# Performance work log

Hardware: AMD Instinct MI355X
Metric: run time of the kernel (lower is better)

The kernel has to match this reference:

```python
import jax, jax.numpy as jnp
import numpy as np

N_NODES = 50000
N_EDGES = 800000
N_RELS = 200
D = 128


def setup_inputs() -> dict:
    key = jax.random.key(0)
    ks = jax.random.split(key, 9)
    h = jax.random.normal(ks[0], (N_NODES, D), dtype=jnp.float32)
    r = jax.random.normal(ks[1], (N_RELS, D), dtype=jnp.float32)
    norm = jax.random.uniform(ks[2], (N_NODES, 1), dtype=jnp.float32)
    src = jax.random.randint(ks[3], (N_EDGES,), 0, N_NODES, dtype=jnp.int32)
    dst = jax.random.randint(ks[4], (N_EDGES,), 0, N_NODES, dtype=jnp.int32)
    rel = jax.random.randint(ks[5], (N_EDGES,), 0, N_RELS, dtype=jnp.int32)
    stdv = 1.0 / np.sqrt(D)
    W_msg = jax.random.uniform(ks[6], (D, D), minval=-stdv, maxval=stdv, dtype=jnp.float32)
    W = jax.random.uniform(ks[7], (D, D), minval=-stdv, maxval=stdv, dtype=jnp.float32)
    b = jax.random.uniform(ks[8], (D,), minval=-stdv, maxval=stdv, dtype=jnp.float32)
    return {"h": h, "r": r, "norm": norm, "src": src, "dst": dst, "rel": rel,
            "W_msg": W_msg, "W": W, "b": b}


def reference(h, r, norm, src, dst, rel, W_msg, W, b):
    # dropout=0.0 (eval); h = h * norm (symmetric-norm pre-scale)
    hn = h * norm                                    # [N, D]
    # per-edge message: (h_src - r_rel) @ W_msg
    msg = (hn[src] - r[rel]) @ W_msg                 # [E, D]
    # scatter-sum to destination nodes, then post-scale by norm
    agg = jax.ops.segment_sum(msg, dst, num_segments=hn.shape[0]) * norm  # [N, D]
    out = hn @ W + agg + b
    return jax.nn.relu(out)
```

## Files before the change

### kernel.cpp

```cpp
#include <hip/hip_runtime.h>

#define N_NODES 50000
#define N_EDGES 800000
#define DIM 128
#define K2 256
#define GN 64
#define NBUCK 196
#define EPB 4096
#define BCAP 16384

typedef unsigned short u16;
typedef __attribute__((ext_vector_type(8))) short short8;
typedef __attribute__((ext_vector_type(4))) float f32x4;

__device__ __forceinline__ float bf2f(u16 v) {
    union { unsigned int u; float f; } x;
    x.u = ((unsigned int)v) << 16;
    return x.f;
}

__device__ __forceinline__ u16 f2bf(float f) {
    union { unsigned int u; float f; } x;
    x.f = f;
    return (u16)((x.u + 0x7FFFu + ((x.u >> 16) & 1u)) >> 16);
}

__global__ void detect_kernel(const void* hraw, int* flag) {
    __shared__ int cnt;
    if (threadIdx.x == 0) cnt = 0;
    __syncthreads();
    const u16* p = (const u16*)hraw;
    u16 v = p[2 * threadIdx.x];
    float a = fabsf(bf2f(v));
    int insane = ((v & 0x7F80) == 0x7F80) || (a != 0.0f && (a > 1e6f || a < 1e-20f));
    if (insane) atomicAdd(&cnt, 1);
    __syncthreads();
    if (threadIdx.x == 0) flag[0] = (cnt > 64) ? 1 : 0;
}

#define PREP_H (N_NODES * 32)
#define PREP_R (200 * 32)
#define PREP_W 8192
__global__ __launch_bounds__(256) void prep_kernel(
    const void* __restrict__ h, const void* __restrict__ r, const void* __restrict__ norm,
    const void* __restrict__ W, const void* __restrict__ Wmsg,
    u16* __restrict__ hx, u16* __restrict__ r_bf, u16* __restrict__ wt,
    const int* __restrict__ flag)
{
    int t = blockIdx.x * 256 + threadIdx.x;
    int isf = flag[0];
    if (t < PREP_H) {
        int n = t >> 5, c = t & 31;
        float4 v; float nv;
        if (isf) {
            nv = ((const float*)norm)[n];
            v = *(const float4*)((const float*)h + (size_t)n * DIM + c * 4);
        } else {
            nv = bf2f(((const u16*)norm)[n]);
            ushort4 u = *(const ushort4*)((const u16*)h + (size_t)n * DIM + c * 4);
            v = make_float4(bf2f(u.x), bf2f(u.y), bf2f(u.z), bf2f(u.w));
        }
        ushort4 o;
        o.x = f2bf(v.x * nv); o.y = f2bf(v.y * nv); o.z = f2bf(v.z * nv); o.w = f2bf(v.w * nv);
        *(ushort4*)(hx + (size_t)n * K2 + c * 4) = o;
    } else if (t < PREP_H + PREP_R) {
        int t2 = t - PREP_H;
        int rho = t2 >> 5, c = t2 & 31;
        float4 v;
        if (isf) v = *(const float4*)((const float*)r + (size_t)rho * DIM + c * 4);
        else {
            ushort4 u = *(const ushort4*)((const u16*)r + (size_t)rho * DIM + c * 4);
            v = make_float4(bf2f(u.x), bf2f(u.y), bf2f(u.z), bf2f(u.w));
        }
        ushort4 o;
        o.x = f2bf(v.x); o.y = f2bf(v.y); o.z = f2bf(v.z); o.w = f2bf(v.w);
        *(ushort4*)(r_bf + (size_t)rho * DIM + c * 4) = o;
    } else if (t < PREP_H + PREP_R + PREP_W) {
        int t3 = t - PREP_H - PREP_R;
        int j = t3 >> 6;
        int k0 = (t3 & 63) * 4;
        ushort4 o;
        u16* op = (u16*)&o;
        for (int kk = 0; kk < 4; ++kk) {
            int k = k0 + kk;
            float wv;
            if (isf) wv = (k < 128) ? ((const float*)W)[(size_t)k * DIM + j]
                                    : ((const float*)Wmsg)[(size_t)(k - 128) * DIM + j];
            else     wv = (k < 128) ? bf2f(((const u16*)W)[(size_t)k * DIM + j])
                                    : bf2f(((const u16*)Wmsg)[(size_t)(k - 128) * DIM + j]);
            op[kk] = f2bf(wv);
        }
        *(ushort4*)(wt + (size_t)j * K2 + k0) = o;
    }
}

__global__ __launch_bounds__(256) void coarse_hist(const int* __restrict__ dst, int* __restrict__ bucketCount) {
    __shared__ int hh[NBUCK];
    for (int i = threadIdx.x; i < NBUCK; i += 256) hh[i] = 0;
    __syncthreads();
    int stride = gridDim.x * 256;
    for (int e = blockIdx.x * 256 + threadIdx.x; e < N_EDGES; e += stride)
        atomicAdd(&hh[dst[e] >> 8], 1);
    __syncthreads();
    for (int i = threadIdx.x; i < NBUCK; i += 256)
        if (hh[i]) atomicAdd(&bucketCount[i], hh[i]);
}

__global__ void bucket_scan(const int* __restrict__ bucketCount,
                            int* __restrict__ bucketBase, int* __restrict__ bucketCursor) {
    __shared__ int sd[256];
    int t = threadIdx.x;
    int c = (t < NBUCK) ? bucketCount[t] : 0;
    sd[t] = c;
    __syncthreads();
    for (int off = 1; off < 256; off <<= 1) {
        int v = (t >= off) ? sd[t - off] : 0;
        __syncthreads();
        sd[t] += v;
        __syncthreads();
    }
    if (t < NBUCK) { int ex = sd[t] - c; bucketBase[t] = ex; bucketCursor[t] = ex; }
    if (t == 0) bucketBase[NBUCK] = N_EDGES;
}

__global__ __launch_bounds__(512) void fill_lds(
    const int* __restrict__ dst, const int* __restrict__ src, const int* __restrict__ rel,
    int* __restrict__ bucketCursor, int* __restrict__ spk)
{
    __shared__ int hist[NBUCK];
    __shared__ int lbase[NBUCK];
    __shared__ int gbase[NBUCK];
    __shared__ int sd[256];
    __shared__ int pay[EPB];
    __shared__ unsigned char bkt[EPB];
    int tid = threadIdx.x;
    for (int i = tid; i < NBUCK; i += 512) hist[i] = 0;
    __syncthreads();
    int e0 = blockIdx.x * EPB;
    int myb[8], myr[8], myp[8];
#pragma unroll
    for (int i = 0; i < 8; ++i) {
        int e = e0 + i * 512 + tid;
        myb[i] = -1;
        if (e < N_EDGES) {
            int d = dst[e];
            int b = d >> 8;
            myb[i] = b;
            myr[i] = atomicAdd(&hist[b], 1);
            myp[i] = src[e] | (rel[e] << 16) | ((d & 255) << 24);
        }
    }
    __syncthreads();
    if (tid < 256) sd[tid] = (tid < NBUCK) ? hist[tid] : 0;
    __syncthreads();
    for (int off = 1; off < 256; off <<= 1) {
        int v = 0;
        if (tid < 256 && tid >= off) v = sd[tid - off];
        __syncthreads();
        if (tid < 256) sd[tid] += v;
        __syncthreads();
    }
    if (tid < NBUCK) {
        lbase[tid] = sd[tid] - hist[tid];
        gbase[tid] = hist[tid] ? atomicAdd(&bucketCursor[tid], hist[tid]) : 0;
    }
    __syncthreads();
#pragma unroll
    for (int i = 0; i < 8; ++i) {
        if (myb[i] >= 0) {
            int lp = lbase[myb[i]] + myr[i];
            pay[lp] = myp[i];
            bkt[lp] = (unsigned char)myb[i];
        }
    }
    __syncthreads();
    int total = N_EDGES - e0; if (total > EPB) total = EPB;
#pragma unroll
    for (int i = 0; i < 8; ++i) {
        int lp = i * 512 + tid;
        if (lp < total) {
            int b = bkt[lp];
            spk[gbase[b] + (lp - lbase[b])] = pay[lp];
        }
    }
}

__global__ __launch_bounds__(256) void node_sort(
    const int* __restrict__ bucketBase, int* __restrict__ spk, int* __restrict__ cursor)
{
    __shared__ int stage[BCAP];
    __shared__ int hist[256];
    __shared__ int nbase[256];
    __shared__ int sd[256];
    int b = blockIdx.x;
    int base = bucketBase[b], end = bucketBase[b + 1];
    int size = end - base; if (size > BCAP) size = BCAP;
    int t = threadIdx.x;
    hist[t] = 0;
    __syncthreads();
    for (int i = t; i < size; i += 256) {
        int pk = spk[base + i];
        stage[i] = pk;
        atomicAdd(&hist[(pk >> 24) & 255], 1);
    }
    __syncthreads();
    int c = hist[t];
    sd[t] = c;
    __syncthreads();
    for (int off = 1; off < 256; off <<= 1) {
        int v = (t >= off) ? sd[t - off] : 0;
        __syncthreads();
        sd[t] += v;
        __syncthreads();
    }
    nbase[t] = sd[t] - c;
    int node = b * 256 + t;
    if (node < N_NODES) cursor[node] = base + sd[t];
    hist[t] = 0;
    __syncthreads();
    for (int i = t; i < size; i += 256) {
        int pk = stage[i];
        int nd = (pk >> 24) & 255;
        int rk = atomicAdd(&hist[nd], 1);
        spk[base + nbase[nd] + rk] = pk;
    }
}

__global__ __launch_bounds__(256) void gather_kernel(
    u16* hx, const u16* __restrict__ r_bf, const void* __restrict__ norm,
    const int* __restrict__ cursor, const int* __restrict__ spk, const int* __restrict__ flag)
{
    int gid = blockIdx.x * 256 + threadIdx.x;
    int n = gid >> 4;
    int g = gid & 15;
    if (n >= N_NODES) return;
    int base = (n == 0) ? 0 : cursor[n - 1];
    int end = cursor[n];
    float acc[8] = {};
    for (int i0 = base; i0 < end; i0 += 16) {
        int my = i0 + g;
        int pk = (my < end) ? spk[my] : 0;
        int m = end - i0; if (m > 16) m = 16;
        int j = 0;
        for (; j + 1 < m; j += 2) {
            int pj0 = __shfl(pk, j, 16);
            int pj1 = __shfl(pk, j + 1, 16);
            int s0 = pj0 & 0xFFFF, r0 = (pj0 >> 16) & 0xFF;
            int s1 = pj1 & 0xFFFF, r1 = (pj1 >> 16) & 0xFF;
            short8 h0 = *(const short8*)(hx + (size_t)s0 * K2 + g * 8);
            short8 v0 = *(const short8*)(r_bf + (size_t)r0 * DIM + g * 8);
            short8 h1 = *(const short8*)(hx + (size_t)s1 * K2 + g * 8);
            short8 v1 = *(const short8*)(r_bf + (size_t)r1 * DIM + g * 8);
#pragma unroll
            for (int d = 0; d < 8; ++d)
                acc[d] += bf2f((u16)h0[d]) - bf2f((u16)v0[d]);
#pragma unroll
            for (int d = 0; d < 8; ++d)
                acc[d] += bf2f((u16)h1[d]) - bf2f((u16)v1[d]);
        }
        if (j < m) {
            int pj = __shfl(pk, j, 16);
            int s = pj & 0xFFFF, rl = (pj >> 16) & 0xFF;
            short8 hv = *(const short8*)(hx + (size_t)s * K2 + g * 8);
            short8 rv = *(const short8*)(r_bf + (size_t)rl * DIM + g * 8);
#pragma unroll
            for (int d = 0; d < 8; ++d)
                acc[d] += bf2f((u16)hv[d]) - bf2f((u16)rv[d]);
        }
    }
    float nv = flag[0] ? ((const float*)norm)[n] : bf2f(((const u16*)norm)[n]);
    short8 o;
#pragma unroll
    for (int d = 0; d < 8; ++d) o[d] = (short)f2bf(acc[d] * nv);
    *(short8*)(hx + (size_t)n * K2 + 128 + g * 8) = o;
}

__global__ __launch_bounds__(256) void mfma_gemm(
    const u16* __restrict__ hx, const u16* __restrict__ wt,
    const void* __restrict__ bias, void* __restrict__ out, const int* __restrict__ flag)
{
    __shared__ u16 X[GN][264];
    int tid = threadIdx.x;
    int nblk = blockIdx.x * GN;

    for (int i = tid; i < GN * 32; i += 256) {
        int nl = i >> 5, c = i & 31;
        int n = nblk + nl;
        short8 v = {0, 0, 0, 0, 0, 0, 0, 0};
        if (n < N_NODES) v = *(const short8*)(hx + (size_t)n * K2 + c * 8);
        *(short8*)&X[nl][c * 8] = v;
    }
    __syncthreads();

    int w = tid >> 6, lane = tid & 63;
    int m = lane & 15, quad = lane >> 4;
    int row0 = w * 16;
    int isf = flag[0];

    short8 a[8];
#pragma unroll
    for (int kb = 0; kb < 8; ++kb)
        a[kb] = *(const short8*)&X[row0 + m][kb * 32 + quad * 8];

#pragma unroll
    for (int ct = 0; ct < 8; ++ct) {
        int n0 = ct * 16;
        f32x4 acc = {0.f, 0.f, 0.f, 0.f};
#pragma unroll
        for (int kb = 0; kb < 8; ++kb) {
            short8 bv = *(const short8*)(wt + (size_t)(n0 + m) * K2 + kb * 32 + quad * 8);
            acc = __builtin_amdgcn_mfma_f32_16x16x32_bf16(a[kb], bv, acc, 0, 0, 0);
        }
        int col = n0 + m;
        float bb = isf ? ((const float*)bias)[col] : bf2f(((const u16*)bias)[col]);
#pragma unroll
        for (int rg = 0; rg < 4; ++rg) {
            int n = nblk + row0 + quad * 4 + rg;
            if (n < N_NODES) {
                float v = acc[rg] + bb;
                v = v > 0.f ? v : 0.f;
                if (isf) ((float*)out)[(size_t)n * DIM + col] = v;
                else     ((u16*)out)[(size_t)n * DIM + col] = f2bf(v);
            }
        }
    }
}

static inline size_t alup(size_t x) { return (x + 255) & ~(size_t)255; }

extern "C" void kernel_launch(void* const* d_in, const int* in_sizes, int n_in,
                              void* d_out, int out_size, void* d_ws, size_t ws_size,
                              hipStream_t stream) {
    const void* h    = d_in[0];
    const void* r    = d_in[1];
    const void* norm = d_in[2];
    const int* src   = (const int*)d_in[3];
    const int* dst   = (const int*)d_in[4];
    const int* rel   = (const int*)d_in[5];
    const void* Wmsg = d_in[6];
    const void* W    = d_in[7];
    const void* b    = d_in[8];

    char* p = (char*)d_ws;
    int* flag     = (int*)p;                 p += 256;
    u16* hx       = (u16*)p;                 p += alup((size_t)N_NODES * K2 * 2);
    u16* r_bf     = (u16*)p;                 p += alup((size_t)200 * DIM * 2);
    u16* wt       = (u16*)p;                 p += alup((size_t)DIM * K2 * 2);
    int* cursor   = (int*)p;                 p += alup((size_t)N_NODES * 4);
    int* bucketCount  = (int*)p;             p += alup((size_t)NBUCK * 4);
    int* bucketBase   = (int*)p;             p += alup((size_t)(NBUCK + 1) * 4);
    int* bucketCursor = (int*)p;             p += alup((size_t)NBUCK * 4);
    int* spk      = (int*)p;                 p += alup((size_t)N_EDGES * 4);

    detect_kernel<<<1, 256, 0, stream>>>(h, flag);
    prep_kernel<<<(PREP_H + PREP_R + PREP_W + 255) / 256, 256, 0, stream>>>(
        h, r, norm, W, Wmsg, hx, r_bf, wt, flag);

    hipMemsetAsync(bucketCount, 0, (size_t)NBUCK * 4, stream);
    coarse_hist<<<128, 256, 0, stream>>>(dst, bucketCount);
    bucket_scan<<<1, 256, 0, stream>>>(bucketCount, bucketBase, bucketCursor);
    fill_lds<<<(N_EDGES + EPB - 1) / EPB, 512, 0, stream>>>(dst, src, rel, bucketCursor, spk);
    node_sort<<<NBUCK, 256, 0, stream>>>(bucketBase, spk, cursor);

    gather_kernel<<<(N_NODES * 16 + 255) / 256, 256, 0, stream>>>(hx, r_bf, norm, cursor, spk, flag);
    mfma_gemm<<<(N_NODES + GN - 1) / GN, 256, 0, stream>>>(hx, wt, b, d_out, flag);
}
```

Before: 198.4 us.

## Fuse detect/prep/hist kernels, inline dtype sniff, stage relation table in LDS

Removes the separate detect kernel by having each block sniff the input dtype with a wavefront ballot. The prep and coarse histogram kernels merge into one launch, and norm and bias are pre-converted to fixed formats. The gather kernel now uses 1024-thread blocks and copies the 200x128 bf16 relation table into LDS, replacing global loads of r with LDS reads. The aim is fewer launches and less global traffic, at the cost of a 51KB LDS load per block, which can lower occupancy.

```diff
diff --git a/kernel.cpp b/kernel.cpp
--- a/kernel.cpp
+++ b/kernel.cpp
@@ -5,6 +5,7 @@
 #define DIM 128
 #define K2 256
 #define GN 64
+#define NREL 200
 #define NBUCK 196
 #define EPB 4096
 #define BCAP 16384
@@ -25,30 +26,44 @@
     return (u16)((x.u + 0x7FFFu + ((x.u >> 16) & 1u)) >> 16);
 }
 
-__global__ void detect_kernel(const void* hraw, int* flag) {
-    __shared__ int cnt;
-    if (threadIdx.x == 0) cnt = 0;
-    __syncthreads();
-    const u16* p = (const u16*)hraw;
-    u16 v = p[2 * threadIdx.x];
+__device__ __forceinline__ int sniff_fp32(const void* h, int tid) {
+    const u16* hp = (const u16*)h;
+    u16 v = hp[2 * (tid & 63)];
     float a = fabsf(bf2f(v));
     int insane = ((v & 0x7F80) == 0x7F80) || (a != 0.0f && (a > 1e6f || a < 1e-20f));
-    if (insane) atomicAdd(&cnt, 1);
-    __syncthreads();
-    if (threadIdx.x == 0) flag[0] = (cnt > 64) ? 1 : 0;
+    return __popcll(__ballot(insane)) > 16;
 }
 
 #define PREP_H (N_NODES * 32)
-#define PREP_R (200 * 32)
+#define PREP_R (NREL * 32)
 #define PREP_W 8192
-__global__ __launch_bounds__(256) void prep_kernel(
+#define PREP_N (N_NODES / 4)
+#define PREP_B 32
+#define PREP_TOT (PREP_H + PREP_R + PREP_W + PREP_N + PREP_B)
+#define PREP_BLOCKS ((PREP_TOT + 255) / 256)
+#define HIST_BLOCKS 128
+__global__ __launch_bounds__(256) void prep_hist(
     const void* __restrict__ h, const void* __restrict__ r, const void* __restrict__ norm,
-    const void* __restrict__ W, const void* __restrict__ Wmsg,
+    const void* __restrict__ W, const void* __restrict__ Wmsg, const void* __restrict__ bias,
+    const int* __restrict__ dst,
     u16* __restrict__ hx, u16* __restrict__ r_bf, u16* __restrict__ wt,
-    const int* __restrict__ flag)
-{
-    int t = blockIdx.x * 256 + threadIdx.x;
-    int isf = flag[0];
+    u16* __restrict__ norm_bf, float* __restrict__ b_f, int* __restrict__ bucketCount)
+{
+    __shared__ int hh[NBUCK];
+    int tid = threadIdx.x;
+    if (blockIdx.x >= PREP_BLOCKS) {
+        for (int i = tid; i < NBUCK; i += 256) hh[i] = 0;
+        __syncthreads();
+        int stride = HIST_BLOCKS * 256;
+        for (int e = (blockIdx.x - PREP_BLOCKS) * 256 + tid; e < N_EDGES; e += stride)
+            atomicAdd(&hh[dst[e] >> 8], 1);
+        __syncthreads();
+        for (int i = tid; i < NBUCK; i += 256)
+            if (hh[i]) atomicAdd(&bucketCount[i], hh[i]);
+        return;
+    }
+    int isf = sniff_fp32(h, tid);
+    int t = blockIdx.x * 256 + tid;
     if (t < PREP_H) {
         int n = t >> 5, c = t & 31;
         float4 v; float nv;
@@ -91,19 +106,26 @@
             op[kk] = f2bf(wv);
         }
         *(ushort4*)(wt + (size_t)j * K2 + k0) = o;
-    }
-}
-
-__global__ __launch_bounds__(256) void coarse_hist(const int* __restrict__ dst, int* __restrict__ bucketCount) {
-    __shared__ int hh[NBUCK];
-    for (int i = threadIdx.x; i < NBUCK; i += 256) hh[i] = 0;
-    __syncthreads();
-    int stride = gridDim.x * 256;
-    for (int e = blockIdx.x * 256 + threadIdx.x; e < N_EDGES; e += stride)
-        atomicAdd(&hh[dst[e] >> 8], 1);
-    __syncthreads();
-    for (int i = threadIdx.x; i < NBUCK; i += 256)
-        if (hh[i]) atomicAdd(&bucketCount[i], hh[i]);
+    } else if (t < PREP_H + PREP_R + PREP_W + PREP_N) {
+        int n0 = (t - PREP_H - PREP_R - PREP_W) * 4;
+        ushort4 o;
+        if (isf) {
+            float4 v = *(const float4*)((const float*)norm + n0);
+            o.x = f2bf(v.x); o.y = f2bf(v.y); o.z = f2bf(v.z); o.w = f2bf(v.w);
+        } else {
+            o = *(const ushort4*)((const u16*)norm + n0);
+        }
+        *(ushort4*)(norm_bf + n0) = o;
+    } else if (t < PREP_TOT) {
+        int j0 = (t - PREP_H - PREP_R - PREP_W - PREP_N) * 4;
+        float4 v;
+        if (isf) v = *(const float4*)((const float*)bias + j0);
+        else {
+            ushort4 u = *(const ushort4*)((const u16*)bias + j0);
+            v = make_float4(bf2f(u.x), bf2f(u.y), bf2f(u.z), bf2f(u.w));
+        }
+        *(float4*)(b_f + j0) = v;
+    }
 }
 
 __global__ void bucket_scan(const int* __restrict__ bucketCount,
@@ -226,11 +248,16 @@
     }
 }
 
-__global__ __launch_bounds__(256) void gather_kernel(
-    u16* hx, const u16* __restrict__ r_bf, const void* __restrict__ norm,
-    const int* __restrict__ cursor, const int* __restrict__ spk, const int* __restrict__ flag)
-{
-    int gid = blockIdx.x * 256 + threadIdx.x;
+__global__ __launch_bounds__(1024) void gather_kernel(
+    u16* hx, const u16* __restrict__ r_bf, const u16* __restrict__ norm_bf,
+    const int* __restrict__ cursor, const int* __restrict__ spk)
+{
+    __shared__ u16 rlds[NREL * DIM];
+    int tid = threadIdx.x;
+    for (int i = tid; i < NREL * DIM / 8; i += 1024)
+        *(short8*)&rlds[i * 8] = *(const short8*)(r_bf + (size_t)i * 8);
+    __syncthreads();
+    int gid = blockIdx.x * 1024 + tid;
     int n = gid >> 4;
     int g = gid & 15;
     if (n >= N_NODES) return;
@@ -248,9 +275,9 @@
             int s0 = pj0 & 0xFFFF, r0 = (pj0 >> 16) & 0xFF;
             int s1 = pj1 & 0xFFFF, r1 = (pj1 >> 16) & 0xFF;
             short8 h0 = *(const short8*)(hx + (size_t)s0 * K2 + g * 8);
-            short8 v0 = *(const short8*)(r_bf + (size_t)r0 * DIM + g * 8);
             short8 h1 = *(const short8*)(hx + (size_t)s1 * K2 + g * 8);
-            short8 v1 = *(const short8*)(r_bf + (size_t)r1 * DIM + g * 8);
+            short8 v0 = *(const short8*)&rlds[r0 * DIM + g * 8];
+            short8 v1 = *(const short8*)&rlds[r1 * DIM + g * 8];
 #pragma unroll
             for (int d = 0; d < 8; ++d)
                 acc[d] += bf2f((u16)h0[d]) - bf2f((u16)v0[d]);
@@ -262,13 +289,13 @@
             int pj = __shfl(pk, j, 16);
             int s = pj & 0xFFFF, rl = (pj >> 16) & 0xFF;
             short8 hv = *(const short8*)(hx + (size_t)s * K2 + g * 8);
-            short8 rv = *(const short8*)(r_bf + (size_t)rl * DIM + g * 8);
+            short8 rv = *(const short8*)&rlds[rl * DIM + g * 8];
 #pragma unroll
             for (int d = 0; d < 8; ++d)
                 acc[d] += bf2f((u16)hv[d]) - bf2f((u16)rv[d]);
         }
     }
-    float nv = flag[0] ? ((const float*)norm)[n] : bf2f(((const u16*)norm)[n]);
+    float nv = bf2f(norm_bf[n]);
     short8 o;
 #pragma unroll
     for (int d = 0; d < 8; ++d) o[d] = (short)f2bf(acc[d] * nv);
@@ -276,12 +303,13 @@
 }
 
 __global__ __launch_bounds__(256) void mfma_gemm(
-    const u16* __restrict__ hx, const u16* __restrict__ wt,
-    const void* __restrict__ bias, void* __restrict__ out, const int* __restrict__ flag)
+    const u16* __restrict__ hx, const u16* __restrict__ wt, const float* __restrict__ b_f,
+    const void* __restrict__ h, void* __restrict__ out)
 {
     __shared__ u16 X[GN][264];
     int tid = threadIdx.x;
     int nblk = blockIdx.x * GN;
+    int isf = sniff_fp32(h, tid);
 
     for (int i = tid; i < GN * 32; i += 256) {
         int nl = i >> 5, c = i & 31;
@@ -295,7 +323,6 @@
     int w = tid >> 6, lane = tid & 63;
     int m = lane & 15, quad = lane >> 4;
     int row0 = w * 16;
-    int isf = flag[0];
 
     short8 a[8];
 #pragma unroll
@@ -312,7 +339,7 @@
             acc = __builtin_amdgcn_mfma_f32_16x16x32_bf16(a[kb], bv, acc, 0, 0, 0);
         }
         int col = n0 + m;
-        float bb = isf ? ((const float*)bias)[col] : bf2f(((const u16*)bias)[col]);
+        float bb = b_f[col];
 #pragma unroll
         for (int rg = 0; rg < 4; ++rg) {
             int n = nblk + row0 + quad * 4 + rg;
@@ -342,26 +369,23 @@
     const void* b    = d_in[8];
 
     char* p = (char*)d_ws;
-    int* flag     = (int*)p;                 p += 256;
     u16* hx       = (u16*)p;                 p += alup((size_t)N_NODES * K2 * 2);
-    u16* r_bf     = (u16*)p;                 p += alup((size_t)200 * DIM * 2);
+    u16* r_bf     = (u16*)p;                 p += alup((size_t)NREL * DIM * 2);
     u16* wt       = (u16*)p;                 p += alup((size_t)DIM * K2 * 2);
+    u16* norm_bf  = (u16*)p;                 p += alup((size_t)N_NODES * 2);
+    float* b_f    = (float*)p;               p += alup((size_t)DIM * 4);
     int* cursor   = (int*)p;                 p += alup((size_t)N_NODES * 4);
     int* bucketCount  = (int*)p;             p += alup((size_t)NBUCK * 4);
     int* bucketBase   = (int*)p;             p += alup((size_t)(NBUCK + 1) * 4);
     int* bucketCursor = (int*)p;             p += alup((size_t)NBUCK * 4);
     int* spk      = (int*)p;                 p += alup((size_t)N_EDGES * 4);
 
-    detect_kernel<<<1, 256, 0, stream>>>(h, flag);
-    prep_kernel<<<(PREP_H + PREP_R + PREP_W + 255) / 256, 256, 0, stream>>>(
-        h, r, norm, W, Wmsg, hx, r_bf, wt, flag);
-
     hipMemsetAsync(bucketCount, 0, (size_t)NBUCK * 4, stream);
-    coarse_hist<<<128, 256, 0, stream>>>(dst, bucketCount);
+    prep_hist<<<PREP_BLOCKS + HIST_BLOCKS, 256, 0, stream>>>(
+        h, r, norm, W, Wmsg, b, dst, hx, r_bf, wt, norm_bf, b_f, bucketCount);
     bucket_scan<<<1, 256, 0, stream>>>(bucketCount, bucketBase, bucketCursor);
     fill_lds<<<(N_EDGES + EPB - 1) / EPB, 512, 0, stream>>>(dst, src, rel, bucketCursor, spk);
     node_sort<<<NBUCK, 256, 0, stream>>>(bucketBase, spk, cursor);
-
-    gather_kernel<<<(N_NODES * 16 + 255) / 256, 256, 0, stream>>>(hx, r_bf, norm, cursor, spk, flag);
-    mfma_gemm<<<(N_NODES + GN - 1) / GN, 256, 0, stream>>>(hx, wt, b, d_out, flag);
-}
+    gather_kernel<<<(N_NODES * 16 + 1023) / 1024, 1024, 0, stream>>>(hx, r_bf, norm_bf, cursor, spk);
+    mfma_gemm<<<(N_NODES + GN - 1) / GN, 256, 0, stream>>>(hx, wt, b_f, h, d_out);
+}
```

After: 199.6 us. No clear change (+0.6%).
